# Kernel optimization log

Measured on AMD Instinct MI355X. Metric: run time of the kernel, lower is better.

## Reference

```python
import jax, jax.numpy as jnp
import numpy as np
import math

D_MODEL, N_HEAD, N_KV_HEAD, MAX_LEN = 2048, 32, 8, 2048
D_K = D_MODEL // N_HEAD
BASE = 10000.0
B, T = 2, 2048


def _rope_tables(seq_len):
    # matches torch Rotary: cos/sin of shape [seq_len, D_K], repeat_interleave(2) over freq dim
    inv_freq = 1.0 / (BASE ** (jnp.arange(0, D_K, 2, dtype=jnp.float32) / D_K))
    t = jnp.arange(seq_len, dtype=jnp.float32)[:, None] * inv_freq  # [T, D_K/2]
    cos = jnp.repeat(jnp.cos(t), 2, axis=-1)  # [T, D_K]
    sin = jnp.repeat(jnp.sin(t), 2, axis=-1)
    return cos, sin


def _rotate_half(x):
    # faithful to source: x1 = even lanes, x2 = odd lanes, concat([-x2, x1], -1)
    x1, x2 = x[..., ::2], x[..., 1::2]
    return jnp.concatenate([-x2, x1], axis=-1)


def _apply_rope(x, cos, sin):
    return x * cos + _rotate_half(x) * sin


def setup_inputs() -> dict:
    key = jax.random.key(0)
    ks = jax.random.split(key, 5)
    s = 1.0 / math.sqrt(D_MODEL)
    x = jax.random.normal(ks[0], (B, T, D_MODEL), dtype=jnp.float32)
    Wq = jax.random.normal(ks[1], (D_MODEL, N_HEAD * D_K), dtype=jnp.float32) * s
    Wk = jax.random.normal(ks[2], (D_MODEL, N_KV_HEAD * D_K), dtype=jnp.float32) * s
    Wv = jax.random.normal(ks[3], (D_MODEL, N_KV_HEAD * D_K), dtype=jnp.float32) * s
    Wo = jax.random.normal(ks[4], (N_HEAD * D_K, D_MODEL), dtype=jnp.float32) * s
    mask = jnp.tril(jnp.ones((T, T), dtype=bool))  # causal
    return {"x": x, "mask": mask, "Wq": Wq, "Wk": Wk, "Wv": Wv, "Wo": Wo}


def reference(x, mask, Wq, Wk, Wv, Wo):
    b, t, _ = x.shape
    g = N_HEAD // N_KV_HEAD
    q = (x @ Wq).reshape(b, t, N_HEAD, D_K).transpose(0, 2, 1, 3)      # [B,H,T,d]
    k = (x @ Wk).reshape(b, t, N_KV_HEAD, D_K).transpose(0, 2, 1, 3)   # [B,Hkv,T,d]
    v = (x @ Wv).reshape(b, t, N_KV_HEAD, D_K).transpose(0, 2, 1, 3)
    cos, sin = _rope_tables(t)
    q = _apply_rope(q, cos, sin)
    k = _apply_rope(k, cos, sin)  # rope before/after repeat is identical per-head
    # grouped attention: q head h attends kv head h // g (repeat_interleave semantics)
    qg = q.reshape(b, N_KV_HEAD, g, t, D_K)
    scores = jnp.einsum("bkgtd,bksd->bkgts", qg, k) / math.sqrt(D_K)
    neg = jnp.finfo(scores.dtype).min
    scores = jnp.where(mask[None, None, None, :, :], scores, neg)
    attn = jax.nn.softmax(scores, axis=-1)
    out = jnp.einsum("bkgts,bksd->bkgtd", attn, v)
    out = out.reshape(b, N_HEAD, t, D_K).transpose(0, 2, 1, 3).reshape(b, t, N_HEAD * D_K)
    return out @ Wo
```

## Files before the change

### kernel.cpp

```cpp
#include <hip/hip_runtime.h>
#include <cstdint>
#include <cstddef>

typedef unsigned short u16;
typedef __attribute__((ext_vector_type(8))) short bf16x8;
typedef __attribute__((ext_vector_type(8))) unsigned short u16x8;
typedef __attribute__((ext_vector_type(4))) unsigned short u16x4;
typedef __attribute__((ext_vector_type(4))) float f32x4;

__device__ __forceinline__ unsigned short f2bf(float f) {
    union { float f; uint32_t u; } c; c.f = f;
    uint32_t u = c.u + 0x7fffu + ((c.u >> 16) & 1u);
    return (unsigned short)(u >> 16);
}
__device__ __forceinline__ float bf2f(unsigned short h) {
    union { uint32_t u; float f; } c; c.u = ((uint32_t)h) << 16;
    return c.f;
}
__device__ __forceinline__ uint32_t cvtpk(float a, float b) {
    uint32_t r;
    asm("v_cvt_pk_bf16_f32 %0, %1, %2" : "=v"(r) : "v"(a), "v"(b));
    return r;
}

#define GLDS16(g, l)                                                               \
    __builtin_amdgcn_global_load_lds((const __attribute__((address_space(1))) void*)(g), \
                                     (__attribute__((address_space(3))) void*)(l), 16, 0, 0)

__global__ __launch_bounds__(256) void cvt_x(const float* __restrict__ src,
                                             u16* __restrict__ dst) {
    int i = blockIdx.x * 256 + threadIdx.x;
    const float4* s = (const float4*)src + (size_t)i * 2;
    float4 a = s[0], b = s[1];
    u16x8 o;
    o[0] = f2bf(a.x); o[1] = f2bf(a.y); o[2] = f2bf(a.z); o[3] = f2bf(a.w);
    o[4] = f2bf(b.x); o[5] = f2bf(b.y); o[6] = f2bf(b.z); o[7] = f2bf(b.w);
    *(u16x8*)(dst + (size_t)i * 8) = o;
}

__global__ __launch_bounds__(256) void tcvt(const float* __restrict__ src,
                                            u16* __restrict__ dst, int C) {
    __shared__ u16 tile[32][33];
    const int t = threadIdx.x;
    const int bx = blockIdx.x, by = blockIdx.y;
    const int tr = t >> 3, tc = (t & 7) << 2;
    float4 f = *(const float4*)&src[(size_t)(by * 32 + tr) * C + bx * 32 + tc];
    tile[tr][tc + 0] = f2bf(f.x); tile[tr][tc + 1] = f2bf(f.y);
    tile[tr][tc + 2] = f2bf(f.z); tile[tr][tc + 3] = f2bf(f.w);
    __syncthreads();
    u16x4 o;
    o[0] = tile[tc + 0][tr]; o[1] = tile[tc + 1][tr];
    o[2] = tile[tc + 2][tr]; o[3] = tile[tc + 3][tr];
    *(u16x4*)&dst[(size_t)(bx * 32 + tr) * 2048 + by * 32 + tc] = o;
}

__global__ __launch_bounds__(256) void tcvt3(const float* __restrict__ Wq,
                                             const float* __restrict__ Wk,
                                             const float* __restrict__ Wv,
                                             u16* __restrict__ dst) {
    __shared__ u16 tile[32][33];
    const int t = threadIdx.x;
    const int bxg = blockIdx.x, by = blockIdx.y;
    const float* src; int C, nb; u16* dbase;
    if (bxg < 64)      { src = Wq; C = 2048; nb = bxg;      dbase = dst; }
    else if (bxg < 80) { src = Wk; C = 512;  nb = bxg - 64; dbase = dst + (size_t)2048 * 2048; }
    else               { src = Wv; C = 512;  nb = bxg - 80; dbase = dst + (size_t)2560 * 2048; }
    const int tr = t >> 3, tc = (t & 7) << 2;
    float4 f = *(const float4*)&src[(size_t)(by * 32 + tr) * C + nb * 32 + tc];
    tile[tr][tc + 0] = f2bf(f.x); tile[tr][tc + 1] = f2bf(f.y);
    tile[tr][tc + 2] = f2bf(f.z); tile[tr][tc + 3] = f2bf(f.w);
    __syncthreads();
    u16x4 o;
    o[0] = tile[tc + 0][tr]; o[1] = tile[tc + 1][tr];
    o[2] = tile[tc + 2][tr]; o[3] = tile[tc + 3][tr];
    *(u16x4*)&dbase[(size_t)(nb * 32 + tr) * 2048 + by * 32 + tc] = o;
}

template <int MODE>
__global__ __launch_bounds__(256) void gemm2(const u16* __restrict__ A,
                                             const u16* __restrict__ Bt,
                                             u16* __restrict__ oq, u16* __restrict__ ok,
                                             u16* __restrict__ ov, float* __restrict__ of) {
    __shared__ u16 As[128 * 32];
    __shared__ u16 Bs[128 * 32];
    const int t = threadIdx.x, w = t >> 6, lane = t & 63;
    const int l15 = lane & 15, quad = lane >> 4;
    const int m0 = blockIdx.y << 7, n0 = blockIdx.x << 7;
    const int K = 2048;
    const int c0 = w * 2, c1 = c0 + 1;
    const int ar0 = c0 * 16 + (lane >> 2), ar1 = c1 * 16 + (lane >> 2);
    const int ac = (lane & 3) << 3;
    const u16* Ap0 = A + (size_t)(m0 + ar0) * K + ac;
    const u16* Ap1 = A + (size_t)(m0 + ar1) * K + ac;
    const u16* Bp0 = Bt + (size_t)(n0 + ar0) * K + ac;
    const u16* Bp1 = Bt + (size_t)(n0 + ar1) * K + ac;
    const int wm = (w >> 1) << 6, wn = (w & 1) << 6;

    f32x4 acc[4][4] = {};

    for (int k0 = 0; k0 < K; k0 += 32) {
        GLDS16(Ap0 + k0, &As[c0 * 512]);
        GLDS16(Ap1 + k0, &As[c1 * 512]);
        GLDS16(Bp0 + k0, &Bs[c0 * 512]);
        GLDS16(Bp1 + k0, &Bs[c1 * 512]);
        __syncthreads();
        bf16x8 a[4], bfr[4];
#pragma unroll
        for (int mt = 0; mt < 4; ++mt)
            a[mt] = *(bf16x8*)&As[(wm + mt * 16 + l15) * 32 + quad * 8];
#pragma unroll
        for (int nt = 0; nt < 4; ++nt)
            bfr[nt] = *(bf16x8*)&Bs[(wn + nt * 16 + l15) * 32 + quad * 8];
#pragma unroll
        for (int mt = 0; mt < 4; ++mt)
#pragma unroll
            for (int nt = 0; nt < 4; ++nt)
                acc[mt][nt] = __builtin_amdgcn_mfma_f32_16x16x32_bf16(a[mt], bfr[nt], acc[mt][nt], 0, 0, 0);
        __syncthreads();
    }

    if constexpr (MODE == 0) {
        const int colbase = n0 + wn;
        const bool isv = (colbase >= 2560);
        float iv[4];
        if (!isv) {
#pragma unroll
            for (int nt = 0; nt < 4; ++nt)
                iv[nt] = exp2f(-0.4152410118609253f * (float)(nt * 8 + (l15 >> 1)));
        }
        const int map1 = (quad << 4) | ((2 * l15 + 1) & 15);
        const int map2 = (quad << 4) | ((2 * l15) & 15);
        const bool lo = (l15 < 8);
#pragma unroll
        for (int mt = 0; mt < 4; ++mt)
#pragma unroll
            for (int r = 0; r < 4; ++r) {
                const int row = m0 + wm + mt * 16 + quad * 4 + r;
                float v0 = acc[mt][0][r], v1 = acc[mt][1][r];
                float v2 = acc[mt][2][r], v3 = acc[mt][3][r];
                float o0 = v0, o1 = v1, o2 = v2, o3 = v3;
                if (!isv) {
                    float g1a = __shfl(v0, map1), g1b = __shfl(v1, map1);
                    float g1c = __shfl(v2, map1), g1d = __shfl(v3, map1);
                    float g2a = __shfl(v0, map2), g2b = __shfl(v1, map2);
                    float g2c = __shfl(v2, map2), g2d = __shfl(v3, map2);
                    float p0 = lo ? g1a : g1b;
                    float p1 = lo ? g1c : g1d;
                    float p2 = lo ? g2a : g2b;
                    float p3 = lo ? g2c : g2d;
                    const float tt = (float)(row & 2047);
                    float sn, cs;
                    __sincosf(tt * iv[0], &sn, &cs); o0 = v0 * cs - p0 * sn;
                    __sincosf(tt * iv[1], &sn, &cs); o1 = v1 * cs - p1 * sn;
                    __sincosf(tt * iv[2], &sn, &cs); o2 = v2 * cs + p2 * sn;
                    __sincosf(tt * iv[3], &sn, &cs); o3 = v3 * cs + p3 * sn;
                }
                float o[4] = {o0, o1, o2, o3};
                if (colbase < 2048) {
#pragma unroll
                    for (int nt = 0; nt < 4; ++nt)
                        oq[(size_t)row * 2048 + colbase + nt * 16 + l15] = f2bf(o[nt]);
                } else if (colbase < 2560) {
#pragma unroll
                    for (int nt = 0; nt < 4; ++nt)
                        ok[(size_t)row * 512 + colbase - 2048 + nt * 16 + l15] = f2bf(o[nt]);
                } else {
#pragma unroll
                    for (int nt = 0; nt < 4; ++nt)
                        ov[(size_t)(colbase - 2560 + nt * 16 + l15) * 4096 + row] = f2bf(o[nt]);
                }
            }
    } else {
#pragma unroll
        for (int mt = 0; mt < 4; ++mt)
#pragma unroll
            for (int nt = 0; nt < 4; ++nt)
#pragma unroll
                for (int r = 0; r < 4; ++r) {
                    int row = m0 + wm + mt * 16 + quad * 4 + r;
                    int col = n0 + wn + nt * 16 + l15;
                    of[(size_t)row * 2048 + col] = acc[mt][nt][r];
                }
    }
}

__global__ __launch_bounds__(512, 4) void attn6(const u16* __restrict__ q,
                                                const u16* __restrict__ k,
                                                const u16* __restrict__ vT,
                                                u16* __restrict__ att) {
    __shared__ u16 Ks[2][64 * 64];
    __shared__ u16 Vt[2][64 * 64];
    __shared__ u16 Pw[8][2][16 * 64];

    const int t = threadIdx.x, w = t >> 6, lane = t & 63;
    const int l15 = lane & 15, quad = lane >> 4;
    const int x = blockIdx.x, kvh = blockIdx.y, z = blockIdx.z;
    const int a = z ? (31 - x) : x;
    const int h = kvh * 4 + (w & 3);
    const int gw = w >> 2;
    const size_t rowbase = (size_t)z * 2048;
    const float SC = 0.125f * 1.4426950408889634f;
    const int swz = l15 & 7;

    const int srow = t >> 3;
    const int slot = t & 7;
    const int sd = slot << 3;
    const int lidx = srow * 64 + ((slot ^ (srow & 7)) << 3);

    const u16* kbase = &k[(rowbase + srow) * 512 + kvh * 64 + sd];
    const u16* vbase = &vT[(size_t)(kvh * 64 + srow) * 4096 + rowbase + sd];

    const int ntiles = a + 1;
    const int qrow0 = a * 64 + gw * 32;

    bf16x8 aq[2][2];
#pragma unroll
    for (int m = 0; m < 2; ++m)
#pragma unroll
        for (int kc = 0; kc < 2; ++kc)
            aq[m][kc] = *(const bf16x8*)&q[(rowbase + qrow0 + m * 16 + l15) * 2048 +
                                           h * 64 + kc * 32 + quad * 8];

    f32x4 acc[2][4] = {};
    float m_i[2] = {-INFINITY, -INFINITY};
    float l_i[2] = {0.f, 0.f};

    u16x8 pk = *(const u16x8*)kbase;
    u16x8 pv = *(const u16x8*)vbase;
    *(u16x8*)&Ks[0][lidx] = pk;
    *(u16x8*)&Vt[0][lidx] = pv;
    if (ntiles > 1) {
        pk = *(const u16x8*)(kbase + (size_t)64 * 512);
        pv = *(const u16x8*)(vbase + 64);
    }
    __syncthreads();

    for (int kb = 0; kb < ntiles; ++kb) {
        const int cur = kb & 1;
        const u16* KsC = &Ks[cur][0];
        const u16* VtC = &Vt[cur][0];

        f32x4 st[2][4] = {};
        __builtin_amdgcn_s_setprio(1);
#pragma unroll
        for (int kt = 0; kt < 4; ++kt) {
            bf16x8 ak0 = *(const bf16x8*)&KsC[(kt * 16 + l15) * 64 + ((quad ^ swz) << 3)];
            bf16x8 ak1 = *(const bf16x8*)&KsC[(kt * 16 + l15) * 64 + (((quad + 4) ^ swz) << 3)];
#pragma unroll
            for (int m = 0; m < 2; ++m) {
                st[m][kt] = __builtin_amdgcn_mfma_f32_16x16x32_bf16(ak0, aq[m][0], st[m][kt], 0, 0, 0);
                st[m][kt] = __builtin_amdgcn_mfma_f32_16x16x32_bf16(ak1, aq[m][1], st[m][kt], 0, 0, 0);
            }
        }
        __builtin_amdgcn_s_setprio(0);

        const bool diag = (kb == ntiles - 1);
        float alpha_[2];
        bool resc[2];
#pragma unroll
        for (int m = 0; m < 2; ++m) {
            float sv[16];
#pragma unroll
            for (int kt = 0; kt < 4; ++kt)
#pragma unroll
                for (int r = 0; r < 4; ++r) sv[kt * 4 + r] = st[m][kt][r];
            if (diag) {
                const int qg = qrow0 + m * 16 + l15;
#pragma unroll
                for (int kt = 0; kt < 4; ++kt)
#pragma unroll
                    for (int r = 0; r < 4; ++r) {
                        int key = kb * 64 + kt * 16 + quad * 4 + r;
                        if (key > qg) sv[kt * 4 + r] = -INFINITY;
                    }
            }
            float mx = sv[0];
#pragma unroll
            for (int i = 1; i < 16; ++i) mx = fmaxf(mx, sv[i]);
            mx = fmaxf(mx, __shfl_xor(mx, 16));
            mx = fmaxf(mx, __shfl_xor(mx, 32));
            mx *= SC;
            const float mold = m_i[m];
            const bool need = __any(mx > mold + 8.f);
            float al = 1.f;
            if (need) {
                const float mnew = fmaxf(mold, mx);
                al = __builtin_amdgcn_exp2f(mold - mnew);
                m_i[m] = mnew;
            }
            const float mu = m_i[m];
            float sum = 0.f;
#pragma unroll
            for (int i = 0; i < 16; ++i) {
                sv[i] = __builtin_amdgcn_exp2f(fmaf(sv[i], SC, -mu));
                sum += sv[i];
            }
            sum += __shfl_xor(sum, 16);
            sum += __shfl_xor(sum, 32);
            l_i[m] = l_i[m] * al + sum;
            alpha_[m] = al;
            resc[m] = need;

            u16* Pq = &Pw[w][m][0];
#pragma unroll
            for (int kt = 0; kt < 4; ++kt) {
                uint2 uu;
                uu.x = cvtpk(sv[kt * 4 + 0], sv[kt * 4 + 1]);
                uu.y = cvtpk(sv[kt * 4 + 2], sv[kt * 4 + 3]);
                *(uint2*)&Pq[l15 * 64 + (((2 * kt + (quad >> 1)) ^ swz) << 3) + ((quad & 1) << 2)] = uu;
            }
        }

        if (kb + 1 < ntiles) {
            *(u16x8*)&Ks[cur ^ 1][lidx] = pk;
            *(u16x8*)&Vt[cur ^ 1][lidx] = pv;
            if (kb + 2 < ntiles) {
                pk = *(const u16x8*)(kbase + (size_t)(kb + 2) * 64 * 512);
                pv = *(const u16x8*)(vbase + (size_t)(kb + 2) * 64);
            }
        }

#pragma unroll
        for (int m = 0; m < 2; ++m)
            if (resc[m]) {
                const float al = alpha_[m];
#pragma unroll
                for (int dt = 0; dt < 4; ++dt)
#pragma unroll
                    for (int r = 0; r < 4; ++r) acc[m][dt][r] *= al;
            }

        bf16x8 bp[2][2];
#pragma unroll
        for (int m = 0; m < 2; ++m) {
            const u16* Pq = &Pw[w][m][0];
            bp[m][0] = *(const bf16x8*)&Pq[l15 * 64 + ((quad ^ swz) << 3)];
            bp[m][1] = *(const bf16x8*)&Pq[l15 * 64 + (((quad + 4) ^ swz) << 3)];
        }

        __builtin_amdgcn_s_setprio(1);
#pragma unroll
        for (int dt = 0; dt < 4; ++dt) {
            bf16x8 av0 = *(const bf16x8*)&VtC[(dt * 16 + l15) * 64 + ((quad ^ swz) << 3)];
            bf16x8 av1 = *(const bf16x8*)&VtC[(dt * 16 + l15) * 64 + (((quad + 4) ^ swz) << 3)];
#pragma unroll
            for (int m = 0; m < 2; ++m) {
                acc[m][dt] = __builtin_amdgcn_mfma_f32_16x16x32_bf16(av0, bp[m][0], acc[m][dt], 0, 0, 0);
                acc[m][dt] = __builtin_amdgcn_mfma_f32_16x16x32_bf16(av1, bp[m][1], acc[m][dt], 0, 0, 0);
            }
        }
        __builtin_amdgcn_s_setprio(0);
        __syncthreads();
    }

#pragma unroll
    for (int m = 0; m < 2; ++m) {
        float inv = 1.0f / l_i[m];
        size_t row = rowbase + qrow0 + m * 16 + l15;
#pragma unroll
        for (int dt = 0; dt < 4; ++dt) {
            uint2 uu;
            uu.x = cvtpk(acc[m][dt][0] * inv, acc[m][dt][1] * inv);
            uu.y = cvtpk(acc[m][dt][2] * inv, acc[m][dt][3] * inv);
            *(uint2*)&att[row * 2048 + h * 64 + dt * 16 + quad * 4] = uu;
        }
    }
}

extern "C" void kernel_launch(void* const* d_in, const int* in_sizes, int n_in,
                              void* d_out, int out_size, void* d_ws, size_t ws_size,
                              hipStream_t stream) {
    const float* x  = (const float*)d_in[0];
    const float* Wq = (const float*)d_in[2];
    const float* Wk = (const float*)d_in[3];
    const float* Wv = (const float*)d_in[4];
    const float* Wo = (const float*)d_in[5];
    float* out = (float*)d_out;

    u16* xb = (u16*)d_out;

    u16* q     = (u16*)d_ws;
    u16* kk    = q + (size_t)4096 * 2048;
    u16* vt    = kk + (size_t)4096 * 512;
    u16* wqkvt = vt + (size_t)4096 * 512;
    u16* att   = wqkvt;
    u16* wot   = kk;

    cvt_x<<<4096, 256, 0, stream>>>(x, xb);
    tcvt3<<<dim3(96, 64), 256, 0, stream>>>(Wq, Wk, Wv, wqkvt);
    gemm2<0><<<dim3(24, 32), 256, 0, stream>>>(xb, wqkvt, q, kk, vt, nullptr);
    attn6<<<dim3(32, 8, 2), 512, 0, stream>>>(q, kk, vt, att);
    tcvt<<<dim3(64, 64), 256, 0, stream>>>(Wo, wot, 2048);
    gemm2<1><<<dim3(16, 32), 256, 0, stream>>>(att, wot, nullptr, nullptr, nullptr, out);
}
```

Measured before the change: 353.4 us.

## Split attention blocks to 32 query rows with 1D heavy-first schedule

The attention kernel now launches 1024 blocks of 256 threads, each handling 32 query rows for the 4 heads of one KV group, instead of 512 blocks of 512 threads covering 64 rows. A 1D grid index is remapped so the longest causal rows are dispatched first and batches and KV heads interleave, aiming at better load balance and more resident blocks. K/V shared memory goes from double buffering to a single buffer, with a register prefetch and two barriers per tile, which halves LDS use but exposes more sync. Each K/V tile is now loaded by more blocks, since half-size blocks reload the same tiles.

```diff
diff --git a/kernel.cpp b/kernel.cpp
--- a/kernel.cpp
+++ b/kernel.cpp
@@ -184,20 +184,29 @@
     }
 }
 
-__global__ __launch_bounds__(512, 4) void attn6(const u16* __restrict__ q,
+__global__ __launch_bounds__(256, 4) void attn7(const u16* __restrict__ q,
                                                 const u16* __restrict__ k,
                                                 const u16* __restrict__ vT,
                                                 u16* __restrict__ att) {
-    __shared__ u16 Ks[2][64 * 64];
-    __shared__ u16 Vt[2][64 * 64];
-    __shared__ u16 Pw[8][2][16 * 64];
+    __shared__ u16 Ks[64 * 64];
+    __shared__ u16 Vt[64 * 64];
+    __shared__ u16 Pw[4][2][16 * 64];
 
     const int t = threadIdx.x, w = t >> 6, lane = t & 63;
     const int l15 = lane & 15, quad = lane >> 4;
-    const int x = blockIdx.x, kvh = blockIdx.y, z = blockIdx.z;
-    const int a = z ? (31 - x) : x;
-    const int h = kvh * 4 + (w & 3);
-    const int gw = w >> 2;
+    const int id = blockIdx.x;
+    const int kvh = id & 7;
+    const int z = (id >> 3) & 1;
+    const int gi = id >> 4;
+    const int p = gi & 15;
+    int g;
+    switch (gi >> 4) {
+        case 0:  g = 63 - p; break;
+        case 1:  g = 32 + p; break;
+        case 2:  g = 31 - p; break;
+        default: g = p;      break;
+    }
+    const int h = kvh * 4 + w;
     const size_t rowbase = (size_t)z * 2048;
     const float SC = 0.125f * 1.4426950408889634f;
     const int swz = l15 & 7;
@@ -210,8 +219,8 @@
     const u16* kbase = &k[(rowbase + srow) * 512 + kvh * 64 + sd];
     const u16* vbase = &vT[(size_t)(kvh * 64 + srow) * 4096 + rowbase + sd];
 
-    const int ntiles = a + 1;
-    const int qrow0 = a * 64 + gw * 32;
+    const int ntiles = (g >> 1) + 1;
+    const int qrow0 = g * 32;
 
     bf16x8 aq[2][2];
 #pragma unroll
@@ -225,27 +234,33 @@
     float m_i[2] = {-INFINITY, -INFINITY};
     float l_i[2] = {0.f, 0.f};
 
-    u16x8 pk = *(const u16x8*)kbase;
-    u16x8 pv = *(const u16x8*)vbase;
-    *(u16x8*)&Ks[0][lidx] = pk;
-    *(u16x8*)&Vt[0][lidx] = pv;
-    if (ntiles > 1) {
-        pk = *(const u16x8*)(kbase + (size_t)64 * 512);
-        pv = *(const u16x8*)(vbase + 64);
-    }
-    __syncthreads();
+    u16x8 pk0 = *(const u16x8*)kbase;
+    u16x8 pk1 = *(const u16x8*)(kbase + (size_t)32 * 512);
+    u16x8 pv0 = *(const u16x8*)vbase;
+    u16x8 pv1 = *(const u16x8*)(vbase + (size_t)32 * 4096);
 
     for (int kb = 0; kb < ntiles; ++kb) {
-        const int cur = kb & 1;
-        const u16* KsC = &Ks[cur][0];
-        const u16* VtC = &Vt[cur][0];
+        __syncthreads();
+        *(u16x8*)&Ks[lidx]        = pk0;
+        *(u16x8*)&Ks[lidx + 2048] = pk1;
+        *(u16x8*)&Vt[lidx]        = pv0;
+        *(u16x8*)&Vt[lidx + 2048] = pv1;
+        if (kb + 1 < ntiles) {
+            const u16* kp = kbase + (size_t)(kb + 1) * 64 * 512;
+            pk0 = *(const u16x8*)kp;
+            pk1 = *(const u16x8*)(kp + (size_t)32 * 512);
+            const u16* vp = vbase + (size_t)(kb + 1) * 64;
+            pv0 = *(const u16x8*)vp;
+            pv1 = *(const u16x8*)(vp + (size_t)32 * 4096);
+        }
+        __syncthreads();
 
         f32x4 st[2][4] = {};
         __builtin_amdgcn_s_setprio(1);
 #pragma unroll
         for (int kt = 0; kt < 4; ++kt) {
-            bf16x8 ak0 = *(const bf16x8*)&KsC[(kt * 16 + l15) * 64 + ((quad ^ swz) << 3)];
-            bf16x8 ak1 = *(const bf16x8*)&KsC[(kt * 16 + l15) * 64 + (((quad + 4) ^ swz) << 3)];
+            bf16x8 ak0 = *(const bf16x8*)&Ks[(kt * 16 + l15) * 64 + ((quad ^ swz) << 3)];
+            bf16x8 ak1 = *(const bf16x8*)&Ks[(kt * 16 + l15) * 64 + (((quad + 4) ^ swz) << 3)];
 #pragma unroll
             for (int m = 0; m < 2; ++m) {
                 st[m][kt] = __builtin_amdgcn_mfma_f32_16x16x32_bf16(ak0, aq[m][0], st[m][kt], 0, 0, 0);
@@ -311,15 +326,6 @@
             }
         }
 
-        if (kb + 1 < ntiles) {
-            *(u16x8*)&Ks[cur ^ 1][lidx] = pk;
-            *(u16x8*)&Vt[cur ^ 1][lidx] = pv;
-            if (kb + 2 < ntiles) {
-                pk = *(const u16x8*)(kbase + (size_t)(kb + 2) * 64 * 512);
-                pv = *(const u16x8*)(vbase + (size_t)(kb + 2) * 64);
-            }
-        }
-
 #pragma unroll
         for (int m = 0; m < 2; ++m)
             if (resc[m]) {
@@ -341,8 +347,8 @@
         __builtin_amdgcn_s_setprio(1);
 #pragma unroll
         for (int dt = 0; dt < 4; ++dt) {
-            bf16x8 av0 = *(const bf16x8*)&VtC[(dt * 16 + l15) * 64 + ((quad ^ swz) << 3)];
-            bf16x8 av1 = *(const bf16x8*)&VtC[(dt * 16 + l15) * 64 + (((quad + 4) ^ swz) << 3)];
+            bf16x8 av0 = *(const bf16x8*)&Vt[(dt * 16 + l15) * 64 + ((quad ^ swz) << 3)];
+            bf16x8 av1 = *(const bf16x8*)&Vt[(dt * 16 + l15) * 64 + (((quad + 4) ^ swz) << 3)];
 #pragma unroll
             for (int m = 0; m < 2; ++m) {
                 acc[m][dt] = __builtin_amdgcn_mfma_f32_16x16x32_bf16(av0, bp[m][0], acc[m][dt], 0, 0, 0);
@@ -350,7 +356,6 @@
             }
         }
         __builtin_amdgcn_s_setprio(0);
-        __syncthreads();
     }
 
 #pragma unroll
@@ -389,7 +394,7 @@
     cvt_x<<<4096, 256, 0, stream>>>(x, xb);
     tcvt3<<<dim3(96, 64), 256, 0, stream>>>(Wq, Wk, Wv, wqkvt);
     gemm2<0><<<dim3(24, 32), 256, 0, stream>>>(xb, wqkvt, q, kk, vt, nullptr);
-    attn6<<<dim3(32, 8, 2), 512, 0, stream>>>(q, kk, vt, att);
+    attn7<<<1024, 256, 0, stream>>>(q, kk, vt, att);
     tcvt<<<dim3(64, 64), 256, 0, stream>>>(Wo, wot, 2048);
     gemm2<1><<<dim3(16, 32), 256, 0, stream>>>(att, wot, nullptr, nullptr, nullptr, out);
 }
```

New measurement: 354.6 us. About the same (+0.3%).
